# Kernel tuning notes

Hardware: AMD Instinct MI355X
Metric: run time of the kernel (lower is better)

## Reference

```python
import jax, jax.numpy as jnp
import numpy as np

N_NODES = 100000
N_EDGES = 600000
D_IN = 128
D_OUT = 128


def setup_inputs() -> dict:
    key = jax.random.key(0)
    k1, k2, k3 = jax.random.split(key, 3)
    x = jax.random.normal(k1, (N_NODES, D_IN), dtype=jnp.float32)
    edge_index = jax.random.randint(k2, (2, N_EDGES), 0, N_NODES, dtype=jnp.int64)
    # Glorot-style init for the GCN weight, zero bias (PyG defaults)
    W = jax.random.normal(k3, (D_IN, D_OUT), dtype=jnp.float32) * (1.0 / np.sqrt(D_IN))
    b = jnp.zeros((D_OUT,), dtype=jnp.float32)
    return {"x": x, "edge_index": edge_index, "W": W, "b": b}


def reference(x, edge_index, W, b):
    """GCNConv: out = D^{-1/2} (A + I) D^{-1/2} (x @ W) + b."""
    n = x.shape[0]
    self_loop = jnp.arange(n, dtype=edge_index.dtype)
    src = jnp.concatenate([edge_index[0], self_loop])  # [E + N]
    dst = jnp.concatenate([edge_index[1], self_loop])

    xw = x @ W  # [N, D_OUT] dense transform before aggregation

    # symmetric normalization with self-loops
    deg = jax.ops.segment_sum(jnp.ones_like(dst, dtype=x.dtype), dst, num_segments=n)
    dinv = jnp.where(deg > 0, jax.lax.rsqrt(deg), 0.0)
    norm = dinv[src] * dinv[dst]  # [E + N]

    # gather source features, scale, scatter-add to destinations
    msgs = norm[:, None] * xw[src]  # [E + N, D_OUT]
    out = jax.ops.segment_sum(msgs, dst, num_segments=n)
    return out + b
```

## Files before the change

kernel.cpp:

```cpp
#include <hip/hip_runtime.h>
#include <hip/hip_bf16.h>
#include <stdint.h>

#define N_NODES 100000
#define N_EDGES 600000
#define D 128
#define WT_LD 136
#define SCAN_NBLK ((N_NODES + 255) / 256)
#define CAP 32

typedef unsigned short u16;
typedef uint32_t u32;
typedef __attribute__((ext_vector_type(8))) short bf16x8;
typedef __attribute__((ext_vector_type(4))) float f32x4;

union bfpack { bf16x8 v; u16 s[8]; };

__device__ __forceinline__ float bf2f(u16 u) {
    union { u32 i; float f; } v; v.i = ((u32)u) << 16; return v.f;
}
__device__ __forceinline__ u16 f2bf(float f) {
    union { float f; u32 i; } v; v.f = f;
    u32 lsb = (v.i >> 16) & 1u;
    return (u16)((v.i + 0x7fffu + lsb) >> 16);
}

__global__ __launch_bounds__(256) void k_init(const u32* __restrict__ xu,
                                              const int* __restrict__ ei,
                                              int* __restrict__ deg,
                                              int* __restrict__ flags) {
    int t = threadIdx.x;
    int idx = blockIdx.x * 256 + t;
    if (idx < N_NODES) deg[idx] = 0;
    if (blockIdx.x == 0) {
        __shared__ int cnt[2];
        if (t < 2) cnt[t] = 0;
        __syncthreads();
        const u32* eu = (const u32*)ei;
        int bad = 0, zc = 0;
        for (int i = 0; i < 16; i++) {
            u32 w = xu[t + 256 * i];
            int e0 = (w >> 7) & 0xFF, e1 = (w >> 23) & 0xFF;
            bad += ((e0 == 0 || e0 == 0xFF) ? 1 : 0) + ((e1 == 0 || e1 == 0xFF) ? 1 : 0);
            zc += (eu[2 * (t + 256 * i) + 1] == 0) ? 1 : 0;
        }
        atomicAdd(&cnt[0], bad);
        atomicAdd(&cnt[1], zc);
        __syncthreads();
        if (t == 0) { flags[0] = cnt[0] > 8 ? 1 : 0; flags[1] = cnt[1] > 2048 ? 1 : 0; }
    }
}

__global__ __launch_bounds__(256) void k_build(const int* __restrict__ ei,
                                               const int* __restrict__ flags,
                                               int* __restrict__ cnt,
                                               int* __restrict__ csr) {
    int t = blockIdx.x * 256 + threadIdx.x;
    if (4 * t >= N_EDGES) return;
    int s[4], d[4];
    if (flags[1]) {
        int4 a0 = *(const int4*)(ei + 8 * t);
        int4 a1 = *(const int4*)(ei + 8 * t + 4);
        int4 b0 = *(const int4*)(ei + 2 * N_EDGES + 8 * t);
        int4 b1 = *(const int4*)(ei + 2 * N_EDGES + 8 * t + 4);
        s[0] = a0.x; s[1] = a0.z; s[2] = a1.x; s[3] = a1.z;
        d[0] = b0.x; d[1] = b0.z; d[2] = b1.x; d[3] = b1.z;
    } else {
        int4 a = *(const int4*)(ei + 4 * t);
        int4 b = *(const int4*)(ei + N_EDGES + 4 * t);
        s[0] = a.x; s[1] = a.y; s[2] = a.z; s[3] = a.w;
        d[0] = b.x; d[1] = b.y; d[2] = b.z; d[3] = b.w;
    }
#pragma unroll
    for (int k = 0; k < 4; k++) {
        int sk = s[k], dk = d[k];
        if ((unsigned)sk >= N_NODES) sk = 0;
        if ((unsigned)dk >= N_NODES) dk = 0;
        int slot = atomicAdd(&cnt[dk], 1);
        if (slot < CAP) csr[(long)dk * CAP + slot] = sk;
    }
}

__global__ void k_hist(const int* __restrict__ ei, const int* __restrict__ flags,
                       int* __restrict__ deg) {
    int e = blockIdx.x * 256 + threadIdx.x;
    if (e < N_EDGES) {
        int d = flags[1] ? ei[2 * (N_EDGES + e)] : ei[N_EDGES + e];
        if ((unsigned)d >= N_NODES) d = 0;
        atomicAdd(&deg[d], 1);
    }
}

__global__ __launch_bounds__(256) void k_reduce(const int* __restrict__ deg,
                                                int* __restrict__ bsum) {
    __shared__ int ws[4];
    int t = threadIdx.x, lane = t & 63, wave = t >> 6;
    int idx = blockIdx.x * 256 + t;
    int v = (idx < N_NODES) ? deg[idx] : 0;
    for (int o = 32; o > 0; o >>= 1) v += __shfl_down(v, o, 64);
    if (lane == 0) ws[wave] = v;
    __syncthreads();
    if (t == 0) bsum[blockIdx.x] = ws[0] + ws[1] + ws[2] + ws[3];
}

__global__ __launch_bounds__(512) void k_scanbs(const int* __restrict__ bsum,
                                                int* __restrict__ bpre,
                                                int* __restrict__ offs) {
    __shared__ int lds[512];
    int t = threadIdx.x;
    int v = (t < SCAN_NBLK) ? bsum[t] : 0;
    lds[t] = v;
    __syncthreads();
    for (int off = 1; off < 512; off <<= 1) {
        int u = (t >= off) ? lds[t - off] : 0;
        __syncthreads();
        lds[t] += u;
        __syncthreads();
    }
    if (t < SCAN_NBLK) bpre[t] = (t == 0) ? 0 : lds[t - 1];
    if (t == SCAN_NBLK - 1) offs[N_NODES] = lds[t];
}

__global__ __launch_bounds__(256) void k_apply(const int* __restrict__ deg,
                                               const int* __restrict__ bpre,
                                               int* __restrict__ offs,
                                               int* __restrict__ cursor) {
    __shared__ int ws[4];
    int t = threadIdx.x, lane = t & 63, wave = t >> 6;
    int idx = blockIdx.x * 256 + t;
    int d = (idx < N_NODES) ? deg[idx] : 0;
    int v = d;
    for (int o = 1; o < 64; o <<= 1) {
        int u = __shfl_up(v, o, 64);
        if (lane >= o) v += u;
    }
    if (lane == 63) ws[wave] = v;
    __syncthreads();
    int add = 0;
    for (int w = 0; w < wave; w++) add += ws[w];
    int excl = bpre[blockIdx.x] + add + v - d;
    if (idx < N_NODES) {
        offs[idx] = excl;
        cursor[idx] = excl;
    }
}

__global__ void k_scatter(const int* __restrict__ ei, const int* __restrict__ flags,
                          int* __restrict__ cursor, int* __restrict__ csr) {
    int e = blockIdx.x * 256 + threadIdx.x;
    if (e < N_EDGES) {
        int s, d;
        if (flags[1]) { s = ei[2 * e]; d = ei[2 * (N_EDGES + e)]; }
        else          { s = ei[e];     d = ei[N_EDGES + e]; }
        if ((unsigned)s >= N_NODES) s = 0;
        if ((unsigned)d >= N_NODES) d = 0;
        int slot = atomicAdd(&cursor[d], 1);
        csr[slot] = s;
    }
}

__global__ __launch_bounds__(256) void k_gemm(const int* __restrict__ flags,
                                              const void* __restrict__ xp,
                                              const void* __restrict__ Wp,
                                              const int* __restrict__ deg,
                                              u16* __restrict__ xw) {
    __shared__ u16 Wt[2][128 * WT_LD];
    int t = threadIdx.x, wave = t >> 6, lane = t & 63;
    int m16 = lane & 15, q = lane >> 4;
    int row0 = blockIdx.x * 128 + wave * 32;
    int f32 = flags[0];
    f32x4 acc[2][8];
    for (int a = 0; a < 2; a++)
        for (int c = 0; c < 8; c++) acc[a][c] = (f32x4){0.f, 0.f, 0.f, 0.f};

    int r0 = row0 + m16;      if (r0 > N_NODES - 1) r0 = N_NODES - 1;
    int r1 = row0 + 16 + m16; if (r1 > N_NODES - 1) r1 = N_NODES - 1;

    if (f32) {
        const float* Wf = (const float*)Wp;
        const float* xf = (const float*)xp;
        for (int i = 0; i < 64; i++) {
            int idx = t + i * 256, k = idx >> 7, n = idx & 127;
            float w = Wf[idx];
            u16 h = f2bf(w);
            Wt[0][n * WT_LD + k] = h;
            Wt[1][n * WT_LD + k] = f2bf(w - bf2f(h));
        }
        __syncthreads();
        for (int kt = 0; kt < 4; kt++) {
            int kbase = kt * 32 + q * 8;
            float4 u0 = *(const float4*)(xf + (long)r0 * D + kbase);
            float4 u1 = *(const float4*)(xf + (long)r0 * D + kbase + 4);
            float4 v0 = *(const float4*)(xf + (long)r1 * D + kbase);
            float4 v1 = *(const float4*)(xf + (long)r1 * D + kbase + 4);
            float t0[8] = {u0.x, u0.y, u0.z, u0.w, u1.x, u1.y, u1.z, u1.w};
            float t1[8] = {v0.x, v0.y, v0.z, v0.w, v1.x, v1.y, v1.z, v1.w};
            bfpack h0, l0, h1, l1;
            for (int j = 0; j < 8; j++) {
                u16 a = f2bf(t0[j]); h0.s[j] = a; l0.s[j] = f2bf(t0[j] - bf2f(a));
                u16 b = f2bf(t1[j]); h1.s[j] = b; l1.s[j] = f2bf(t1[j] - bf2f(b));
            }
            for (int ct = 0; ct < 8; ct++) {
                bf16x8 bh = *(const bf16x8*)(&Wt[0][(ct * 16 + m16) * WT_LD + kbase]);
                bf16x8 bl = *(const bf16x8*)(&Wt[1][(ct * 16 + m16) * WT_LD + kbase]);
                acc[0][ct] = __builtin_amdgcn_mfma_f32_16x16x32_bf16(h0.v, bh, acc[0][ct], 0, 0, 0);
                acc[0][ct] = __builtin_amdgcn_mfma_f32_16x16x32_bf16(l0.v, bh, acc[0][ct], 0, 0, 0);
                acc[0][ct] = __builtin_amdgcn_mfma_f32_16x16x32_bf16(h0.v, bl, acc[0][ct], 0, 0, 0);
                acc[1][ct] = __builtin_amdgcn_mfma_f32_16x16x32_bf16(h1.v, bh, acc[1][ct], 0, 0, 0);
                acc[1][ct] = __builtin_amdgcn_mfma_f32_16x16x32_bf16(l1.v, bh, acc[1][ct], 0, 0, 0);
                acc[1][ct] = __builtin_amdgcn_mfma_f32_16x16x32_bf16(h1.v, bl, acc[1][ct], 0, 0, 0);
            }
        }
    } else {
        const u16* W16 = (const u16*)Wp;
        const u16* x16 = (const u16*)xp;
        for (int i = 0; i < 64; i++) {
            int idx = t + i * 256, k = idx >> 7, n = idx & 127;
            Wt[0][n * WT_LD + k] = W16[idx];
        }
        __syncthreads();
        for (int kt = 0; kt < 4; kt++) {
            int kbase = kt * 32 + q * 8;
            bf16x8 a0 = *(const bf16x8*)(x16 + (long)r0 * D + kbase);
            bf16x8 a1 = *(const bf16x8*)(x16 + (long)r1 * D + kbase);
            for (int ct = 0; ct < 8; ct++) {
                bf16x8 b = *(const bf16x8*)(&Wt[0][(ct * 16 + m16) * WT_LD + kbase]);
                acc[0][ct] = __builtin_amdgcn_mfma_f32_16x16x32_bf16(a0, b, acc[0][ct], 0, 0, 0);
                acc[1][ct] = __builtin_amdgcn_mfma_f32_16x16x32_bf16(a1, b, acc[1][ct], 0, 0, 0);
            }
        }
    }
    for (int a = 0; a < 2; a++)
        for (int r = 0; r < 4; r++) {
            int row = row0 + a * 16 + q * 4 + r;
            if (row < N_NODES) {
                float dr = rsqrtf((float)(deg[row] + 1));
                for (int ct = 0; ct < 8; ct++)
                    xw[(long)row * D + ct * 16 + m16] = f2bf(dr * acc[a][ct][r]);
            }
        }
}

__global__ __launch_bounds__(256) void k_agg_bkt(const int* __restrict__ flags,
                                                 const u16* __restrict__ xw,
                                                 const int* __restrict__ csr,
                                                 const int* __restrict__ cnt,
                                                 const void* __restrict__ bp,
                                                 void* __restrict__ outp) {
    int t = threadIdx.x;
    int wave = t >> 6, lane = t & 63;
    int g = lane >> 4, i = lane & 15;
    int nb = blockIdx.x * 16 + wave * 4;
    int n = nb + g;

    int4 dv = *(const int4*)(cnt + nb);
    int deg = (g == 0) ? dv.x : (g == 1) ? dv.y : (g == 2) ? dv.z : dv.w;
    float dn = rsqrtf((float)(deg + 1));
    int m = deg < CAP ? deg : CAP;
    int rounds = (m + 3) >> 2;
    float padf = (float)(1 - (rounds * 4 - m));

    const u16* xwc = xw + i * 8;
    bfpack pv; pv.v = *(const bf16x8*)(xwc + (long)n * D);
    float ax[8];
#pragma unroll
    for (int j2 = 0; j2 < 8; j2++) ax[j2] = bf2f(pv.s[j2]) * padf;

    const int* base = csr + (long)n * CAP;
    for (int j = 0; j < m; j += 4) {
        int4 qi = *(const int4*)(base + j);
        int s0 = qi.x;
        int s1 = (j + 1 < m) ? qi.y : n;
        int s2 = (j + 2 < m) ? qi.z : n;
        int s3 = (j + 3 < m) ? qi.w : n;
        bfpack g0, g1, g2, g3;
        g0.v = *(const bf16x8*)(xwc + (long)s0 * D);
        g1.v = *(const bf16x8*)(xwc + (long)s1 * D);
        g2.v = *(const bf16x8*)(xwc + (long)s2 * D);
        g3.v = *(const bf16x8*)(xwc + (long)s3 * D);
#pragma unroll
        for (int j2 = 0; j2 < 8; j2++)
            ax[j2] += (bf2f(g0.s[j2]) + bf2f(g1.s[j2])) +
                      (bf2f(g2.s[j2]) + bf2f(g3.s[j2]));
    }

    if (flags[0]) {
        const float* bf_ = (const float*)bp;
        f32x4 b0 = *(const f32x4*)(bf_ + i * 8);
        f32x4 b1 = *(const f32x4*)(bf_ + i * 8 + 4);
        f32x4 o0, o1;
#pragma unroll
        for (int j2 = 0; j2 < 4; j2++) {
            o0[j2] = dn * ax[j2] + b0[j2];
            o1[j2] = dn * ax[j2 + 4] + b1[j2];
        }
        float* outf = (float*)outp;
        *(f32x4*)(outf + (long)n * D + i * 8) = o0;
        *(f32x4*)(outf + (long)n * D + i * 8 + 4) = o1;
    } else {
        const u16* b16 = (const u16*)bp;
        bfpack bb; bb.v = *(const bf16x8*)(b16 + i * 8);
        bfpack ob;
#pragma unroll
        for (int j2 = 0; j2 < 8; j2++) ob.s[j2] = f2bf(dn * ax[j2] + bf2f(bb.s[j2]));
        u16* out16 = (u16*)outp;
        *(bf16x8*)(out16 + (long)n * D + i * 8) = ob.v;
    }
}

__global__ __launch_bounds__(256) void k_agg_csr(const int* __restrict__ flags,
                                                 const u16* __restrict__ xw,
                                                 const int* __restrict__ csr,
                                                 const int* __restrict__ offs,
                                                 const void* __restrict__ bp,
                                                 void* __restrict__ outp) {
    int wave = threadIdx.x >> 6, lane = threadIdx.x & 63;
    int n = blockIdx.x * 4 + wave;
    int c = lane * 2;
    int e0 = offs[n], e1 = offs[n + 1];
    float dn = rsqrtf((float)(e1 - e0 + 1));
    u32 pv = *(const u32*)(xw + (long)n * D + c);
    float ax = bf2f((u16)pv), ay = bf2f((u16)(pv >> 16));
    int j = e0;
    for (; j + 4 <= e1; j += 4) {
        int s0 = csr[j], s1 = csr[j + 1], s2 = csr[j + 2], s3 = csr[j + 3];
        u32 q0 = *(const u32*)(xw + (long)s0 * D + c);
        u32 q1 = *(const u32*)(xw + (long)s1 * D + c);
        u32 q2 = *(const u32*)(xw + (long)s2 * D + c);
        u32 q3 = *(const u32*)(xw + (long)s3 * D + c);
        ax += bf2f((u16)q0) + bf2f((u16)q1) + bf2f((u16)q2) + bf2f((u16)q3);
        ay += bf2f((u16)(q0 >> 16)) + bf2f((u16)(q1 >> 16)) +
              bf2f((u16)(q2 >> 16)) + bf2f((u16)(q3 >> 16));
    }
    for (; j < e1; j++) {
        int s = csr[j];
        u32 qv = *(const u32*)(xw + (long)s * D + c);
        ax += bf2f((u16)qv);
        ay += bf2f((u16)(qv >> 16));
    }
    if (flags[0]) {
        const float* bf_ = (const float*)bp;
        float2 bb = *(const float2*)(bf_ + c);
        float* outf = (float*)outp;
        *(float2*)(outf + (long)n * D + c) = make_float2(dn * ax + bb.x, dn * ay + bb.y);
    } else {
        const u16* b16 = (const u16*)bp;
        u32 bb = *(const u32*)(b16 + c);
        u16* out16 = (u16*)outp;
        u32 o = (u32)f2bf(dn * ax + bf2f((u16)bb)) |
                ((u32)f2bf(dn * ay + bf2f((u16)(bb >> 16))) << 16);
        *(u32*)(out16 + (long)n * D + c) = o;
    }
}

extern "C" void kernel_launch(void* const* d_in, const int* in_sizes, int n_in,
                              void* d_out, int out_size, void* d_ws, size_t ws_size,
                              hipStream_t stream) {
    const void* x  = d_in[0];
    const int* ei  = (const int*)d_in[1];
    const void* W  = d_in[2];
    const void* b  = d_in[3];
    char* ws = (char*)d_ws;

    const size_t BUCKET_NEED = 64 + 400000 + (size_t)N_NODES * CAP * 4 + (size_t)N_NODES * D * 2 + 64;
    if (ws_size >= BUCKET_NEED) {
        int* flags = (int*)(ws + 0);
        int* cnt   = (int*)(ws + 64);
        int* csr   = (int*)(ws + 400128);
        u16* xw    = (u16*)(ws + 400128 + (size_t)N_NODES * CAP * 4);
        k_init<<<SCAN_NBLK, 256, 0, stream>>>((const u32*)x, ei, cnt, flags);
        k_build<<<(N_EDGES / 4 + 255) / 256, 256, 0, stream>>>(ei, flags, cnt, csr);
        k_gemm<<<(N_NODES + 127) / 128, 256, 0, stream>>>(flags, x, W, cnt, xw);
        k_agg_bkt<<<N_NODES / 16, 256, 0, stream>>>(flags, xw, csr, cnt, b, d_out);
    } else {
        int*   flags  = (int*)(ws + 0);
        int*   deg    = (int*)(ws + 64);
        int*   offs   = (int*)(ws + 400064);
        int*   cursor = (int*)(ws + 800068);
        int*   csr    = (int*)(ws + 1200068);
        int*   bsum   = (int*)(ws + 3600068);
        int*   bpre   = (int*)(ws + 3601636);
        u16*   xw     = (u16*)(ws + 3603216);
        k_init<<<SCAN_NBLK, 256, 0, stream>>>((const u32*)x, ei, deg, flags);
        k_hist<<<(N_EDGES + 255) / 256, 256, 0, stream>>>(ei, flags, deg);
        k_reduce<<<SCAN_NBLK, 256, 0, stream>>>(deg, bsum);
        k_scanbs<<<1, 512, 0, stream>>>(bsum, bpre, offs);
        k_apply<<<SCAN_NBLK, 256, 0, stream>>>(deg, bpre, offs, cursor);
        k_gemm<<<(N_NODES + 127) / 128, 256, 0, stream>>>(flags, x, W, deg, xw);
        k_scatter<<<(N_EDGES + 255) / 256, 256, 0, stream>>>(ei, flags, cursor, csr);
        k_agg_csr<<<N_NODES / 4, 256, 0, stream>>>(flags, xw, csr, offs, b, d_out);
    }
}
```

Before: 203.6 us.

## Precompute transposed bf16 weight split once and read it from global in GEMM

```diff
diff --git a/kernel.cpp b/kernel.cpp
--- a/kernel.cpp
+++ b/kernel.cpp
@@ -5,7 +5,6 @@
 #define N_NODES 100000
 #define N_EDGES 600000
 #define D 128
-#define WT_LD 136
 #define SCAN_NBLK ((N_NODES + 255) / 256)
 #define CAP 32
 
@@ -51,34 +50,44 @@
     }
 }
 
+__global__ __launch_bounds__(256) void k_prep(const int* __restrict__ flags,
+                                              const void* __restrict__ Wp,
+                                              u16* __restrict__ wthi,
+                                              u16* __restrict__ wtlo) {
+    int t = blockIdx.x * 256 + threadIdx.x;
+    if (flags[0]) {
+        const float* Wf = (const float*)Wp;
+        for (int i = 0; i < 8; i++) {
+            int idx = t + i * 2048;
+            float w = Wf[idx];
+            int k = idx >> 7, n = idx & 127;
+            u16 h = f2bf(w);
+            wthi[n * 128 + k] = h;
+            wtlo[n * 128 + k] = f2bf(w - bf2f(h));
+        }
+    } else {
+        const u16* W16 = (const u16*)Wp;
+        for (int i = 0; i < 8; i++) {
+            int idx = t + i * 2048;
+            int k = idx >> 7, n = idx & 127;
+            wthi[n * 128 + k] = W16[idx];
+        }
+    }
+}
+
 __global__ __launch_bounds__(256) void k_build(const int* __restrict__ ei,
                                                const int* __restrict__ flags,
                                                int* __restrict__ cnt,
                                                int* __restrict__ csr) {
-    int t = blockIdx.x * 256 + threadIdx.x;
-    if (4 * t >= N_EDGES) return;
-    int s[4], d[4];
-    if (flags[1]) {
-        int4 a0 = *(const int4*)(ei + 8 * t);
-        int4 a1 = *(const int4*)(ei + 8 * t + 4);
-        int4 b0 = *(const int4*)(ei + 2 * N_EDGES + 8 * t);
-        int4 b1 = *(const int4*)(ei + 2 * N_EDGES + 8 * t + 4);
-        s[0] = a0.x; s[1] = a0.z; s[2] = a1.x; s[3] = a1.z;
-        d[0] = b0.x; d[1] = b0.z; d[2] = b1.x; d[3] = b1.z;
-    } else {
-        int4 a = *(const int4*)(ei + 4 * t);
-        int4 b = *(const int4*)(ei + N_EDGES + 4 * t);
-        s[0] = a.x; s[1] = a.y; s[2] = a.z; s[3] = a.w;
-        d[0] = b.x; d[1] = b.y; d[2] = b.z; d[3] = b.w;
-    }
-#pragma unroll
-    for (int k = 0; k < 4; k++) {
-        int sk = s[k], dk = d[k];
-        if ((unsigned)sk >= N_NODES) sk = 0;
-        if ((unsigned)dk >= N_NODES) dk = 0;
-        int slot = atomicAdd(&cnt[dk], 1);
-        if (slot < CAP) csr[(long)dk * CAP + slot] = sk;
-    }
+    int e = blockIdx.x * 256 + threadIdx.x;
+    if (e >= N_EDGES) return;
+    int s, d;
+    if (flags[1]) { s = ei[2 * e]; d = ei[2 * (N_EDGES + e)]; }
+    else          { s = ei[e];     d = ei[N_EDGES + e]; }
+    if ((unsigned)s >= N_NODES) s = 0;
+    if ((unsigned)d >= N_NODES) d = 0;
+    int slot = atomicAdd(&cnt[d], 1);
+    if (slot < CAP) csr[(long)d * CAP + slot] = s;
 }
 
 __global__ void k_hist(const int* __restrict__ ei, const int* __restrict__ flags,
@@ -161,14 +170,13 @@
 
 __global__ __launch_bounds__(256) void k_gemm(const int* __restrict__ flags,
                                               const void* __restrict__ xp,
-                                              const void* __restrict__ Wp,
+                                              const u16* __restrict__ wthi,
+                                              const u16* __restrict__ wtlo,
                                               const int* __restrict__ deg,
                                               u16* __restrict__ xw) {
-    __shared__ u16 Wt[2][128 * WT_LD];
     int t = threadIdx.x, wave = t >> 6, lane = t & 63;
     int m16 = lane & 15, q = lane >> 4;
     int row0 = blockIdx.x * 128 + wave * 32;
-    int f32 = flags[0];
     f32x4 acc[2][8];
     for (int a = 0; a < 2; a++)
         for (int c = 0; c < 8; c++) acc[a][c] = (f32x4){0.f, 0.f, 0.f, 0.f};
@@ -176,17 +184,8 @@
     int r0 = row0 + m16;      if (r0 > N_NODES - 1) r0 = N_NODES - 1;
     int r1 = row0 + 16 + m16; if (r1 > N_NODES - 1) r1 = N_NODES - 1;
 
-    if (f32) {
-        const float* Wf = (const float*)Wp;
+    if (flags[0]) {
         const float* xf = (const float*)xp;
-        for (int i = 0; i < 64; i++) {
-            int idx = t + i * 256, k = idx >> 7, n = idx & 127;
-            float w = Wf[idx];
-            u16 h = f2bf(w);
-            Wt[0][n * WT_LD + k] = h;
-            Wt[1][n * WT_LD + k] = f2bf(w - bf2f(h));
-        }
-        __syncthreads();
         for (int kt = 0; kt < 4; kt++) {
             int kbase = kt * 32 + q * 8;
             float4 u0 = *(const float4*)(xf + (long)r0 * D + kbase);
@@ -201,8 +200,8 @@
                 u16 b = f2bf(t1[j]); h1.s[j] = b; l1.s[j] = f2bf(t1[j] - bf2f(b));
             }
             for (int ct = 0; ct < 8; ct++) {
-                bf16x8 bh = *(const bf16x8*)(&Wt[0][(ct * 16 + m16) * WT_LD + kbase]);
-                bf16x8 bl = *(const bf16x8*)(&Wt[1][(ct * 16 + m16) * WT_LD + kbase]);
+                bf16x8 bh = *(const bf16x8*)(wthi + (ct * 16 + m16) * 128 + kbase);
+                bf16x8 bl = *(const bf16x8*)(wtlo + (ct * 16 + m16) * 128 + kbase);
                 acc[0][ct] = __builtin_amdgcn_mfma_f32_16x16x32_bf16(h0.v, bh, acc[0][ct], 0, 0, 0);
                 acc[0][ct] = __builtin_amdgcn_mfma_f32_16x16x32_bf16(l0.v, bh, acc[0][ct], 0, 0, 0);
                 acc[0][ct] = __builtin_amdgcn_mfma_f32_16x16x32_bf16(h0.v, bl, acc[0][ct], 0, 0, 0);
@@ -212,19 +211,13 @@
             }
         }
     } else {
-        const u16* W16 = (const u16*)Wp;
         const u16* x16 = (const u16*)xp;
-        for (int i = 0; i < 64; i++) {
-            int idx = t + i * 256, k = idx >> 7, n = idx & 127;
-            Wt[0][n * WT_LD + k] = W16[idx];
-        }
-        __syncthreads();
         for (int kt = 0; kt < 4; kt++) {
             int kbase = kt * 32 + q * 8;
             bf16x8 a0 = *(const bf16x8*)(x16 + (long)r0 * D + kbase);
             bf16x8 a1 = *(const bf16x8*)(x16 + (long)r1 * D + kbase);
             for (int ct = 0; ct < 8; ct++) {
-                bf16x8 b = *(const bf16x8*)(&Wt[0][(ct * 16 + m16) * WT_LD + kbase]);
+                bf16x8 b = *(const bf16x8*)(wthi + (ct * 16 + m16) * 128 + kbase);
                 acc[0][ct] = __builtin_amdgcn_mfma_f32_16x16x32_bf16(a0, b, acc[0][ct], 0, 0, 0);
                 acc[1][ct] = __builtin_amdgcn_mfma_f32_16x16x32_bf16(a1, b, acc[1][ct], 0, 0, 0);
             }
@@ -362,15 +355,18 @@
     const void* b  = d_in[3];
     char* ws = (char*)d_ws;
 
-    const size_t BUCKET_NEED = 64 + 400000 + (size_t)N_NODES * CAP * 4 + (size_t)N_NODES * D * 2 + 64;
+    const size_t BUCKET_NEED = 38865664 + 64;
     if (ws_size >= BUCKET_NEED) {
         int* flags = (int*)(ws + 0);
         int* cnt   = (int*)(ws + 64);
         int* csr   = (int*)(ws + 400128);
-        u16* xw    = (u16*)(ws + 400128 + (size_t)N_NODES * CAP * 4);
+        u16* xw    = (u16*)(ws + 13200128);
+        u16* wthi  = (u16*)(ws + 38800128);
+        u16* wtlo  = (u16*)(ws + 38832896);
         k_init<<<SCAN_NBLK, 256, 0, stream>>>((const u32*)x, ei, cnt, flags);
-        k_build<<<(N_EDGES / 4 + 255) / 256, 256, 0, stream>>>(ei, flags, cnt, csr);
-        k_gemm<<<(N_NODES + 127) / 128, 256, 0, stream>>>(flags, x, W, cnt, xw);
+        k_build<<<(N_EDGES + 255) / 256, 256, 0, stream>>>(ei, flags, cnt, csr);
+        k_prep<<<8, 256, 0, stream>>>(flags, W, wthi, wtlo);
+        k_gemm<<<(N_NODES + 127) / 128, 256, 0, stream>>>(flags, x, wthi, wtlo, cnt, xw);
         k_agg_bkt<<<N_NODES / 16, 256, 0, stream>>>(flags, xw, csr, cnt, b, d_out);
     } else {
         int*   flags  = (int*)(ws + 0);
@@ -381,12 +377,15 @@
         int*   bsum   = (int*)(ws + 3600068);
         int*   bpre   = (int*)(ws + 3601636);
         u16*   xw     = (u16*)(ws + 3603216);
+        u16*   wthi   = (u16*)(ws + 29203264);
+        u16*   wtlo   = (u16*)(ws + 29236032);
         k_init<<<SCAN_NBLK, 256, 0, stream>>>((const u32*)x, ei, deg, flags);
         k_hist<<<(N_EDGES + 255) / 256, 256, 0, stream>>>(ei, flags, deg);
         k_reduce<<<SCAN_NBLK, 256, 0, stream>>>(deg, bsum);
         k_scanbs<<<1, 512, 0, stream>>>(bsum, bpre, offs);
         k_apply<<<SCAN_NBLK, 256, 0, stream>>>(deg, bpre, offs, cursor);
-        k_gemm<<<(N_NODES + 127) / 128, 256, 0, stream>>>(flags, x, W, deg, xw);
+        k_prep<<<8, 256, 0, stream>>>(flags, W, wthi, wtlo);
+        k_gemm<<<(N_NODES + 127) / 128, 256, 0, stream>>>(flags, x, wthi, wtlo, deg, xw);
         k_scatter<<<(N_EDGES + 255) / 256, 256, 0, stream>>>(ei, flags, cursor, csr);
         k_agg_csr<<<N_NODES / 4, 256, 0, stream>>>(flags, xw, csr, offs, b, d_out);
     }
```

Result: slower. 211.4 us (+3.9%).
